# Kernel tuning notes

Hardware: AMD Instinct MI355X
Metric: run time of the kernel (lower is better)

## Reference

```python
import jax, jax.numpy as jnp
import numpy as np

SHAPES = ((92, 160), (46, 80), (23, 40), (12, 20))  # multi-scale (H, W) per level
B, NQ, C, M, P = 8, 900, 256, 8, 4
L = len(SHAPES)
D = C // M          # head dim = 32
S = sum(h * w for h, w in SHAPES)  # 19560 flattened keys
NC = 10
FFN = 1024


def setup_inputs() -> dict:
    key = jax.random.key(0)
    ks = jax.random.split(key, 16)
    f = lambda k, sh, s=0.02: jax.random.normal(k, sh, dtype=jnp.float32) * s
    return dict(
        query=jax.random.normal(ks[0], (B, NQ, C), dtype=jnp.float32),
        value=jax.random.normal(ks[1], (B, S, C), dtype=jnp.float32),
        ref_points=jax.random.uniform(ks[2], (B, NQ, 2), dtype=jnp.float32),
        w_value=f(ks[3], (C, C)), b_value=jnp.zeros((C,), jnp.float32),
        w_off=f(ks[4], (C, M * L * P * 2)), b_off=f(ks[5], (M * L * P * 2,), 0.5),
        w_attn=f(ks[6], (C, M * L * P)), b_attn=jnp.zeros((M * L * P,), jnp.float32),
        w_out=f(ks[7], (C, C)), b_out=jnp.zeros((C,), jnp.float32),
        ln1_w=jnp.ones((C,), jnp.float32), ln1_b=jnp.zeros((C,), jnp.float32),
        w_ffn1=f(ks[8], (C, FFN)), b_ffn1=jnp.zeros((FFN,), jnp.float32),
        w_ffn2=f(ks[9], (FFN, C)), b_ffn2=jnp.zeros((C,), jnp.float32),
        ln2_w=jnp.ones((C,), jnp.float32), ln2_b=jnp.zeros((C,), jnp.float32),
        w_cls=f(ks[10], (C, NC)), b_cls=jnp.zeros((NC,), jnp.float32),
    )


def _ln(x, w, b, eps=1e-6):
    u = x.mean(-1, keepdims=True)
    s = ((x - u) ** 2).mean(-1, keepdims=True)
    return (x - u) * jax.lax.rsqrt(s + eps) * w + b


def _sample_level(v_l, loc, Hl, Wl):
    # v_l: [B, Hl*Wl, M, D] level features; loc: [B, NQ, M, P, 2] normalized sampling locations.
    # Bilinear interpolation with zero padding (grid_sample align_corners=False convention).
    x = loc[..., 0] * Wl - 0.5
    y = loc[..., 1] * Hl - 0.5
    x0 = jnp.floor(x)
    y0 = jnp.floor(y)
    lx, ly = x - x0, y - y0
    vt = jnp.transpose(v_l, (0, 2, 1, 3))  # [B, M, S_l, D]

    def gather(xi, yi):
        valid = ((xi >= 0) & (xi < Wl) & (yi >= 0) & (yi < Hl)).astype(v_l.dtype)
        idx = (jnp.clip(yi, 0, Hl - 1) * Wl + jnp.clip(xi, 0, Wl - 1)).astype(jnp.int32)
        idx = jnp.transpose(idx, (0, 2, 1, 3)).reshape(B, M, NQ * P)
        g = jnp.take_along_axis(vt, idx[..., None], axis=2).reshape(B, M, NQ, P, D)
        return g * jnp.transpose(valid, (0, 2, 1, 3))[..., None]

    x0i, y0i = x0.astype(jnp.int32), y0.astype(jnp.int32)
    g00 = gather(x0i, y0i)
    g01 = gather(x0i + 1, y0i)
    g10 = gather(x0i, y0i + 1)
    g11 = gather(x0i + 1, y0i + 1)
    wx = jnp.transpose(lx, (0, 2, 1, 3))[..., None]
    wy = jnp.transpose(ly, (0, 2, 1, 3))[..., None]
    return g00 * (1 - wx) * (1 - wy) + g01 * wx * (1 - wy) + g10 * (1 - wx) * wy + g11 * wx * wy


def reference(query, value, ref_points, w_value, b_value, w_off, b_off, w_attn, b_attn,
              w_out, b_out, ln1_w, ln1_b, w_ffn1, b_ffn1, w_ffn2, b_ffn2, ln2_w, ln2_b,
              w_cls, b_cls):
    v = (value @ w_value + b_value).reshape(B, S, M, D)
    off = (query @ w_off + b_off).reshape(B, NQ, M, L, P, 2)
    attn = jax.nn.softmax((query @ w_attn + b_attn).reshape(B, NQ, M, L * P), axis=-1)
    attn = attn.reshape(B, NQ, M, L, P)
    norm = jnp.asarray([[w, h] for h, w in SHAPES], dtype=query.dtype)  # [L, 2] (W, H)
    loc = ref_points[:, :, None, None, None, :] + off / norm[None, None, None, :, None, :]

    out = jnp.zeros((B, M, NQ, D), dtype=query.dtype)
    start = 0
    for l, (Hl, Wl) in enumerate(SHAPES):
        v_l = jax.lax.dynamic_slice_in_dim(v, start, Hl * Wl, axis=1)
        samp = _sample_level(v_l, loc[:, :, :, l], Hl, Wl)          # [B, M, NQ, P, D]
        a = jnp.transpose(attn[:, :, :, l], (0, 2, 1, 3))[..., None]  # [B, M, NQ, P, 1]
        out = out + (samp * a).sum(3)
        start += Hl * Wl

    feat = jnp.transpose(out, (0, 2, 1, 3)).reshape(B, NQ, C) @ w_out + b_out
    x = _ln(query + feat, ln1_w, ln1_b)
    h = jax.nn.relu(x @ w_ffn1 + b_ffn1) @ w_ffn2 + b_ffn2
    x = _ln(x + h, ln2_w, ln2_b)
    return x @ w_cls + b_cls
```

## Files before the change

### kernel.cpp

```cpp
#include <hip/hip_runtime.h>
#include <cstddef>
#include <cstdint>

#define B_    8
#define NQ_   900
#define C_    256
#define M_    8
#define P_    4
#define L_    4
#define D_    32
#define S_    19560
#define NC_   10
#define FFN_  1024
#define RQ_   (B_ * NQ_)
#define RV_   (B_ * S_)

typedef __attribute__((ext_vector_type(8))) short bf8_t;
typedef __attribute__((ext_vector_type(8))) unsigned short us8_t;
typedef __attribute__((ext_vector_type(4))) float f4_t;
typedef unsigned short ushort_t;

__device__ __forceinline__ unsigned short f2bf(float x) {
    union { float f; unsigned u; } v; v.f = x;
    unsigned r = v.u + 0x7FFF + ((v.u >> 16) & 1);
    return (unsigned short)(r >> 16);
}
__device__ __forceinline__ float bfu2f(unsigned short u) {
    union { unsigned u; float f; } v; v.u = ((unsigned)u) << 16; return v.f;
}

__global__ __launch_bounds__(256) void prep_weights(
    const float* __restrict__ w_value, const float* __restrict__ w_off,
    const float* __restrict__ w_attn,  const float* __restrict__ w_out,
    const float* __restrict__ w_ffn1,  const float* __restrict__ w_ffn2,
    short* __restrict__ WvT, short* __restrict__ WoaT, short* __restrict__ WoutT,
    short* __restrict__ Wf1T, short* __restrict__ Wf2T)
{
    const int mat = blockIdx.z;
    int K, N; const float* src; short* dst;
    switch (mat) {
        case 0: K = 256;  N = 256;  src = w_value; dst = WvT;  break;
        case 1: K = 256;  N = 384;  src = nullptr; dst = WoaT; break;
        case 2: K = 256;  N = 256;  src = w_out;   dst = WoutT; break;
        case 3: K = 256;  N = 1024; src = w_ffn1;  dst = Wf1T; break;
        default:K = 1024; N = 256;  src = w_ffn2;  dst = Wf2T; break;
    }
    const int ntn = N >> 6;
    const int kt = blockIdx.x / ntn, nt = blockIdx.x % ntn;
    if (kt >= (K >> 6)) return;

    __shared__ float t[64][65];
    const int tx = threadIdx.x & 63;
    const int ty = threadIdx.x >> 6;
#pragma unroll
    for (int i = 0; i < 64; i += 4) {
        const int k = kt * 64 + i + ty;
        const int n = nt * 64 + tx;
        float v;
        if (mat == 1) v = (n < 256) ? w_off[(size_t)k * 256 + n]
                                    : w_attn[(size_t)k * 128 + (n - 256)];
        else          v = src[(size_t)k * N + n];
        t[i + ty][tx] = v;
    }
    __syncthreads();
#pragma unroll
    for (int i = 0; i < 64; i += 4) {
        const int n = nt * 64 + i + ty;
        const int k = kt * 64 + tx;
        dst[(size_t)n * K + k] = (short)f2bf(t[tx][i + ty]);
    }
}

__global__ __launch_bounds__(384) void prep_bias(
    const float* __restrict__ b_off, const float* __restrict__ b_attn,
    float* __restrict__ bias_cat)
{
    const int t = threadIdx.x;
    bias_cat[t] = (t < 256) ? b_off[t] : b_attn[t - 256];
}

__global__ __launch_bounds__(512, 4) void gemm_value(
    const float* __restrict__ A, const short* __restrict__ WT,
    const float* __restrict__ bias, ushort_t* __restrict__ outv, int R)
{
    __shared__ __align__(16) char smem[49152];
    short* As = (short*)smem;
    short* Bs = (short*)(smem + 16384);

    const int tid  = threadIdx.x;
    const int lane = tid & 63;
    const int wave = tid >> 6;
    const int wr   = wave >> 2;
    const int wc   = wave & 3;
    const int g    = lane >> 4;
    const int fr   = lane & 15;

    const int row0 = blockIdx.x * 128;

    const int r_base = tid >> 3;
    const int ku     = tid & 7;

    float4 rA[2][2];
#pragma unroll
    for (int it = 0; it < 2; ++it) {
        rA[it][0] = make_float4(0.f, 0.f, 0.f, 0.f);
        rA[it][1] = make_float4(0.f, 0.f, 0.f, 0.f);
    }
    int4 rB[4];
    f4_t acc[4][4] = {};

    auto LOAD = [&](int k0) {
#pragma unroll
        for (int it = 0; it < 2; ++it) {
            const int grow = row0 + it * 64 + r_base;
            if (grow < R) {
                rA[it][0] = *(const float4*)(A + (size_t)grow * 256 + k0 + ku * 8);
                rA[it][1] = *(const float4*)(A + (size_t)grow * 256 + k0 + ku * 8 + 4);
            }
        }
#pragma unroll
        for (int it = 0; it < 4; ++it) {
            const int n = it * 64 + r_base;
            rB[it] = *(const int4*)(WT + (size_t)n * 256 + k0 + ku * 8);
        }
    };
    auto WRITE = [&]() {
#pragma unroll
        for (int it = 0; it < 2; ++it) {
            const int r = it * 64 + r_base;
            const float va[8] = {rA[it][0].x, rA[it][0].y, rA[it][0].z, rA[it][0].w,
                                 rA[it][1].x, rA[it][1].y, rA[it][1].z, rA[it][1].w};
            bf8_t pk;
#pragma unroll
            for (int j = 0; j < 8; ++j) pk[j] = (short)f2bf(va[j]);
            *(bf8_t*)&As[r * 64 + (ku ^ (r & 7)) * 8] = pk;
        }
#pragma unroll
        for (int it = 0; it < 4; ++it) {
            const int n = it * 64 + r_base;
            *(int4*)&Bs[n * 64 + (ku ^ (n & 7)) * 8] = rB[it];
        }
    };

    LOAD(0);
    for (int k0 = 0; k0 < 256; k0 += 64) {
        WRITE();
        __syncthreads();
        if (k0 + 64 < 256) LOAD(k0 + 64);
#pragma unroll
        for (int c = 0; c < 2; ++c) {
            bf8_t fa[4], fb[4];
#pragma unroll
            for (int i = 0; i < 4; ++i) {
                const int ar = wr * 64 + i * 16 + fr;
                fa[i] = *(const bf8_t*)&As[ar * 64 + ((c * 4 + g) ^ (ar & 7)) * 8];
            }
#pragma unroll
            for (int j = 0; j < 4; ++j) {
                const int br = wc * 64 + j * 16 + fr;
                fb[j] = *(const bf8_t*)&Bs[br * 64 + ((c * 4 + g) ^ (br & 7)) * 8];
            }
#pragma unroll
            for (int i = 0; i < 4; ++i)
#pragma unroll
                for (int j = 0; j < 4; ++j)
                    acc[i][j] = __builtin_amdgcn_mfma_f32_16x16x32_bf16(
                        fa[i], fb[j], acc[i][j], 0, 0, 0);
        }
        __syncthreads();
    }

    ushort_t* eps = (ushort_t*)smem;
    for (int h = 0; h < 2; ++h) {
        __syncthreads();
        if ((wc >> 1) == h) {
            const int wcl = wc & 1;
#pragma unroll
            for (int j = 0; j < 4; ++j) {
                const int col_l = wcl * 64 + j * 16 + fr;
                const float bcol = bias[h * 128 + col_l];
#pragma unroll
                for (int i = 0; i < 4; ++i)
#pragma unroll
                    for (int r = 0; r < 4; ++r) {
                        const int row_l = wr * 64 + i * 16 + g * 4 + r;
                        eps[row_l * 136 + col_l] = f2bf(acc[i][j][r] + bcol);
                    }
            }
        }
        __syncthreads();
#pragma unroll
        for (int u = 0; u < 4; ++u) {
            const int unit = u * 512 + tid;
            const int sl = unit >> 4;
            const int cc = unit & 15;
            const int grow = row0 + sl;
            if (grow < R) {
                const int b = grow / S_;
                const int s = grow - b * S_;
                const int col = h * 128 + cc * 8;
                const int m = col >> 5;
                const int d = col & 31;
                *(int4*)&outv[(((size_t)(b * M_ + m)) * S_ + s) * D_ + d] =
                    *(const int4*)&eps[sl * 136 + cc * 8];
            }
        }
    }
}

template <int MODE, int BM>
__global__ __launch_bounds__(256) void gemm_mfma(
    const float* __restrict__ A, const short* __restrict__ WT,
    const float* __restrict__ bias, const float* __restrict__ res,
    float* __restrict__ out, int R, int N, int K)
{
    constexpr int NI  = BM / 32;
    constexpr int AIT = BM * 8 / 256;
    constexpr int ASB = BM * 128;
    constexpr int SMEM_BYTES = ASB + 16384;

    __shared__ __align__(16) char smem[SMEM_BYTES];
    short* As = (short*)smem;
    short* Bs = (short*)(smem + ASB);

    const int tid  = threadIdx.x;
    const int lane = tid & 63;
    const int wave = tid >> 6;
    const int wr   = wave >> 1;
    const int wc   = wave & 1;
    const int g    = lane >> 4;
    const int fr   = lane & 15;

    const int row0 = blockIdx.x * BM;
    const int col0 = blockIdx.y * 128;

    const int r_base = tid >> 3;
    const int ku     = tid & 7;

    float4 rA[AIT][2];
#pragma unroll
    for (int it = 0; it < AIT; ++it) {
        rA[it][0] = make_float4(0.f, 0.f, 0.f, 0.f);
        rA[it][1] = make_float4(0.f, 0.f, 0.f, 0.f);
    }
    int4 rB[4];

    f4_t acc[NI][4] = {};

    auto LOAD = [&](int k0) {
#pragma unroll
        for (int it = 0; it < AIT; ++it) {
            const int grow = row0 + it * 32 + r_base;
            if (grow < R) {
                rA[it][0] = *(const float4*)(A + (size_t)grow * K + k0 + ku * 8);
                rA[it][1] = *(const float4*)(A + (size_t)grow * K + k0 + ku * 8 + 4);
            }
        }
#pragma unroll
        for (int it = 0; it < 4; ++it) {
            const int n = it * 32 + r_base;
            rB[it] = *(const int4*)(WT + (size_t)(col0 + n) * K + k0 + ku * 8);
        }
    };
    auto WRITE = [&]() {
#pragma unroll
        for (int it = 0; it < AIT; ++it) {
            const int r = it * 32 + r_base;
            const float va[8] = {rA[it][0].x, rA[it][0].y, rA[it][0].z, rA[it][0].w,
                                 rA[it][1].x, rA[it][1].y, rA[it][1].z, rA[it][1].w};
            bf8_t pk;
#pragma unroll
            for (int j = 0; j < 8; ++j) pk[j] = (short)f2bf(va[j]);
            *(bf8_t*)&As[r * 64 + (ku ^ (r & 7)) * 8] = pk;
        }
#pragma unroll
        for (int it = 0; it < 4; ++it) {
            const int n = it * 32 + r_base;
            *(int4*)&Bs[n * 64 + (ku ^ (n & 7)) * 8] = rB[it];
        }
    };

    LOAD(0);
    for (int k0 = 0; k0 < K; k0 += 64) {
        WRITE();
        __syncthreads();
        if (k0 + 64 < K) LOAD(k0 + 64);
#pragma unroll
        for (int c = 0; c < 2; ++c) {
            bf8_t fa[NI], fb[4];
#pragma unroll
            for (int i = 0; i < NI; ++i) {
                const int ar = wr * (BM / 2) + i * 16 + fr;
                fa[i] = *(const bf8_t*)&As[ar * 64 + ((c * 4 + g) ^ (ar & 7)) * 8];
            }
#pragma unroll
            for (int j = 0; j < 4; ++j) {
                const int br = wc * 64 + j * 16 + fr;
                fb[j] = *(const bf8_t*)&Bs[br * 64 + ((c * 4 + g) ^ (br & 7)) * 8];
            }
#pragma unroll
            for (int i = 0; i < NI; ++i)
#pragma unroll
                for (int j = 0; j < 4; ++j)
                    acc[i][j] = __builtin_amdgcn_mfma_f32_16x16x32_bf16(
                        fa[i], fb[j], acc[i][j], 0, 0, 0);
        }
        __syncthreads();
    }

#pragma unroll
    for (int j = 0; j < 4; ++j) {
        const int col = col0 + wc * 64 + j * 16 + fr;
        const float bcol = bias[col];
#pragma unroll
        for (int i = 0; i < NI; ++i) {
#pragma unroll
            for (int r = 0; r < 4; ++r) {
                const int row = row0 + wr * (BM / 2) + i * 16 + g * 4 + r;
                if (row >= R) continue;
                float vv = acc[i][j][r] + bcol;
                if (MODE == 2) {
                    out[(size_t)row * N + col] = fmaxf(vv, 0.f);
                } else if (MODE == 3) {
                    out[(size_t)row * N + col] = vv + res[(size_t)row * N + col];
                } else {
                    out[(size_t)row * N + col] = vv;
                }
            }
        }
    }
}

__global__ __launch_bounds__(128) void softmax_loc_kernel(
    const float* __restrict__ oa, const float* __restrict__ ref,
    float* __restrict__ loc, float* __restrict__ attn)
{
    const int row = blockIdx.x;
    const int t   = threadIdx.x;
    const float Wtab[L_] = {160.f, 80.f, 40.f, 20.f};
    const float Htab[L_] = {92.f, 46.f, 23.f, 12.f};

    float vlog = oa[(size_t)row * 384 + 256 + t];
    float mx = vlog;
#pragma unroll
    for (int o = 8; o >= 1; o >>= 1) mx = fmaxf(mx, __shfl_xor(mx, o, 64));
    const float e = __expf(vlog - mx);
    float sm = e;
#pragma unroll
    for (int o = 8; o >= 1; o >>= 1) sm += __shfl_xor(sm, o, 64);
    attn[(size_t)row * 128 + t] = e / sm;

    const int m = t >> 4, l = (t >> 2) & 3, p = t & 3;
    const float rx = ref[(size_t)row * 2 + 0];
    const float ry = ref[(size_t)row * 2 + 1];
    const int oi = m * 32 + l * 8 + p * 2;
    loc[(size_t)row * 256 + oi + 0] = rx * Wtab[l] + oa[(size_t)row * 384 + oi + 0] - 0.5f;
    loc[(size_t)row * 256 + oi + 1] = ry * Htab[l] + oa[(size_t)row * 384 + oi + 1] - 0.5f;
}

__global__ __launch_bounds__(256) void sample_kernel(
    const ushort_t* __restrict__ v, const float* __restrict__ loc,
    const float* __restrict__ attn, float* __restrict__ outf)
{
    const int row0 = blockIdx.x * 8;
    const int t    = threadIdx.x;
    const int rl   = t >> 5;
    const int m    = (t >> 2) & 7;
    const int dg   = t & 3;

    __shared__ float sloc[8][8][33];
    __shared__ float satt[8][8][17];

    {
        const float4* src = (const float4*)(loc + (size_t)row0 * 256);
#pragma unroll
        for (int i = 0; i < 2; ++i) {
            const int u   = i * 256 + t;
            const int r_  = u >> 6;
            const int rem = u & 63;
            const int m_  = rem >> 3;
            const int c4  = (rem & 7) * 4;
            *(float4*)&sloc[r_][m_][c4] = src[u];
        }
        const float4* asrc = (const float4*)(attn + (size_t)row0 * 128);
        {
            const int u   = t;
            const int r_  = u >> 5;
            const int rem = u & 31;
            const int m_  = rem >> 2;
            const int c4  = (rem & 3) * 4;
            *(float4*)&satt[r_][m_][c4] = asrc[u];
        }
    }
    __syncthreads();

    const int row = row0 + rl;
    const int b   = row / NQ_;
    const ushort_t* vbase = v + (((size_t)(b * M_ + m)) * S_) * D_ + dg * 8;

    const int Wtab[L_] = {160, 80, 40, 20};
    const int Htab[L_] = {92, 46, 23, 12};
    const int Stab[L_] = {0, 14720, 18400, 19320};

    float acc[8] = {};

#pragma unroll
    for (int l = 0; l < L_; ++l) {
        const int Wl = Wtab[l], Hl = Htab[l], st = Stab[l];
#pragma unroll
        for (int p = 0; p < P_; ++p) {
            const float x = sloc[rl][m][l * 8 + p * 2 + 0];
            const float y = sloc[rl][m][l * 8 + p * 2 + 1];
            const float a = satt[rl][m][l * 4 + p];
            const float xf = floorf(x), yf = floorf(y);
            const int x0 = (int)xf, y0 = (int)yf;
            const float lx = x - xf, ly = y - yf;
            const float wx0 = (x0 >= 0 && x0 < Wl)         ? (1.f - lx) : 0.f;
            const float wx1 = (x0 + 1 >= 0 && x0 + 1 < Wl) ? lx         : 0.f;
            const float wy0 = (y0 >= 0 && y0 < Hl)         ? (1.f - ly) : 0.f;
            const float wy1 = (y0 + 1 >= 0 && y0 + 1 < Hl) ? ly         : 0.f;
            const float ay0 = a * wy0, ay1 = a * wy1;
            const float aw00 = ay0 * wx0, aw01 = ay0 * wx1;
            const float aw10 = ay1 * wx0, aw11 = ay1 * wx1;
            const int xc0 = min(max(x0, 0), Wl - 1);
            const int xc1 = min(max(x0 + 1, 0), Wl - 1);
            const int yc0 = min(max(y0, 0), Hl - 1);
            const int yc1 = min(max(y0 + 1, 0), Hl - 1);
            const us8_t s00 = *(const us8_t*)(vbase + (size_t)(st + yc0 * Wl + xc0) * D_);
            const us8_t s01 = *(const us8_t*)(vbase + (size_t)(st + yc0 * Wl + xc1) * D_);
            const us8_t s10 = *(const us8_t*)(vbase + (size_t)(st + yc1 * Wl + xc0) * D_);
            const us8_t s11 = *(const us8_t*)(vbase + (size_t)(st + yc1 * Wl + xc1) * D_);
#pragma unroll
            for (int j = 0; j < 8; ++j)
                acc[j] += aw00 * bfu2f(s00[j]) + aw01 * bfu2f(s01[j])
                        + aw10 * bfu2f(s10[j]) + aw11 * bfu2f(s11[j]);
        }
    }

    float* o = outf + (size_t)row * 256 + m * 32 + dg * 8;
    *(float4*)o       = make_float4(acc[0], acc[1], acc[2], acc[3]);
    *((float4*)o + 1) = make_float4(acc[4], acc[5], acc[6], acc[7]);
}

__global__ __launch_bounds__(64) void ln_kernel(
    const float* __restrict__ in, const float* __restrict__ w,
    const float* __restrict__ bp, float* __restrict__ out)
{
    const int row  = blockIdx.x;
    const int lane = threadIdx.x;
    const float4 x = ((const float4*)(in + (size_t)row * C_))[lane];
    float s = x.x + x.y + x.z + x.w;
#pragma unroll
    for (int o = 32; o >= 1; o >>= 1) s += __shfl_xor(s, o, 64);
    const float mean = s * (1.f / C_);
    const float d0 = x.x - mean, d1 = x.y - mean, d2 = x.z - mean, d3 = x.w - mean;
    float ss = d0 * d0 + d1 * d1 + d2 * d2 + d3 * d3;
#pragma unroll
    for (int o = 32; o >= 1; o >>= 1) ss += __shfl_xor(ss, o, 64);
    const float r = rsqrtf(ss * (1.f / C_) + 1e-6f);
    const float4 wv = ((const float4*)w)[lane];
    const float4 bv = ((const float4*)bp)[lane];
    float4 o4;
    o4.x = d0 * r * wv.x + bv.x;
    o4.y = d1 * r * wv.y + bv.y;
    o4.z = d2 * r * wv.z + bv.z;
    o4.w = d3 * r * wv.w + bv.w;
    ((float4*)(out + (size_t)row * C_))[lane] = o4;
}

__global__ __launch_bounds__(64) void cls_kernel(
    const float* __restrict__ x, const float* __restrict__ w,
    const float* __restrict__ bias, float* __restrict__ out)
{
    const int row  = blockIdx.x;
    const int lane = threadIdx.x;
    float acc[NC_] = {};
#pragma unroll
    for (int j = 0; j < 4; ++j) {
        const int k = lane + j * 64;
        const float xk = x[(size_t)row * C_ + k];
        const float* wr = w + (size_t)k * NC_;
#pragma unroll
        for (int n = 0; n < NC_; ++n) acc[n] += xk * wr[n];
    }
#pragma unroll
    for (int n = 0; n < NC_; ++n) {
        float s = acc[n];
#pragma unroll
        for (int o = 32; o >= 1; o >>= 1) s += __shfl_xor(s, o, 64);
        if (lane == n) out[(size_t)row * NC_ + n] = s + bias[n];
    }
}

extern "C" void kernel_launch(void* const* d_in, const int* in_sizes, int n_in,
                              void* d_out, int out_size, void* d_ws, size_t ws_size,
                              hipStream_t stream)
{
    const float* query   = (const float*)d_in[0];
    const float* value   = (const float*)d_in[1];
    const float* refp    = (const float*)d_in[2];
    const float* w_value = (const float*)d_in[3];
    const float* b_value = (const float*)d_in[4];
    const float* w_off   = (const float*)d_in[5];
    const float* b_off   = (const float*)d_in[6];
    const float* w_attn  = (const float*)d_in[7];
    const float* b_attn  = (const float*)d_in[8];
    const float* w_out   = (const float*)d_in[9];
    const float* b_out   = (const float*)d_in[10];
    const float* ln1w    = (const float*)d_in[11];
    const float* ln1b    = (const float*)d_in[12];
    const float* w_ffn1  = (const float*)d_in[13];
    const float* b_ffn1  = (const float*)d_in[14];
    const float* w_ffn2  = (const float*)d_in[15];
    const float* b_ffn2  = (const float*)d_in[16];
    const float* ln2w    = (const float*)d_in[17];
    const float* ln2b    = (const float*)d_in[18];
    const float* w_cls   = (const float*)d_in[19];
    const float* b_cls   = (const float*)d_in[20];

    short* WvT   = (short*)d_ws;
    short* WoaT  = WvT  + 65536;
    short* WoutT = WoaT + 98304;
    short* Wf1T  = WoutT + 65536;
    short* Wf2T  = Wf1T + 262144;
    float* bias_cat = (float*)(Wf2T + 262144);
    ushort_t* v = (ushort_t*)(bias_cat + 384);
    float* oa   = (float*)(v + (size_t)RV_ * C_);
    float* loc  = oa   + (size_t)RQ_ * 384;
    float* attn = loc  + (size_t)RQ_ * 256;
    float* feat = attn + (size_t)RQ_ * 128;
    float* tmp  = feat + (size_t)RQ_ * 256;
    float* h    = tmp  + (size_t)RQ_ * 256;
    float* x2   = h    + (size_t)RQ_ * FFN_;

    prep_weights<<<dim3(64, 1, 5), 256, 0, stream>>>(
        w_value, w_off, w_attn, w_out, w_ffn1, w_ffn2,
        WvT, WoaT, WoutT, Wf1T, Wf2T);
    prep_bias<<<1, 384, 0, stream>>>(b_off, b_attn, bias_cat);

    gemm_value<<<(RV_ + 127) / 128, 512, 0, stream>>>(
        value, WvT, b_value, v, RV_);

    gemm_mfma<0, 64><<<dim3((RQ_ + 63) / 64, 3), 256, 0, stream>>>(
        query, WoaT, bias_cat, nullptr, oa, RQ_, 384, 256);

    softmax_loc_kernel<<<RQ_, 128, 0, stream>>>(oa, refp, loc, attn);

    sample_kernel<<<RQ_ / 8, 256, 0, stream>>>(v, loc, attn, feat);

    gemm_mfma<3, 64><<<dim3((RQ_ + 63) / 64, 2), 256, 0, stream>>>(
        feat, WoutT, b_out, query, tmp, RQ_, 256, 256);

    ln_kernel<<<RQ_, 64, 0, stream>>>(tmp, ln1w, ln1b, feat);

    gemm_mfma<2, 64><<<dim3((RQ_ + 63) / 64, 8), 256, 0, stream>>>(
        feat, Wf1T, b_ffn1, nullptr, h, RQ_, 1024, 256);

    gemm_mfma<3, 64><<<dim3((RQ_ + 63) / 64, 2), 256, 0, stream>>>(
        h, Wf2T, b_ffn2, feat, tmp, RQ_, 256, 1024);

    ln_kernel<<<RQ_, 64, 0, stream>>>(tmp, ln2w, ln2b, x2);

    cls_kernel<<<RQ_, 64, 0, stream>>>(x2, w_cls, b_cls, (float*)d_out);
}
```

Baseline: 493.6 us.

## Shrink value GEMM tile to 64 rows with double-buffered A prefetch

The value-projection GEMM now uses 64-row tiles instead of 128, which halves the A shared-memory buffer and the accumulator count, and raises the occupancy hint to 6 blocks. The K loop is fully unrolled, and A loads are prefetched two stages ahead into alternating register buffers. The epilogue writes the whole 256-column tile at once, without the two-half pass. This targets better latency hiding and occupancy on the memory-bound value GEMM, at the cost of more loads of B per row and removing the row bounds check on A loads (RV is divisible by 64).

```diff
diff --git a/kernel.cpp b/kernel.cpp
--- a/kernel.cpp
+++ b/kernel.cpp
@@ -79,13 +79,13 @@
     bias_cat[t] = (t < 256) ? b_off[t] : b_attn[t - 256];
 }
 
-__global__ __launch_bounds__(512, 4) void gemm_value(
+__global__ __launch_bounds__(512, 6) void gemm_value(
     const float* __restrict__ A, const short* __restrict__ WT,
     const float* __restrict__ bias, ushort_t* __restrict__ outv, int R)
 {
-    __shared__ __align__(16) char smem[49152];
+    __shared__ __align__(16) char smem[40960];
     short* As = (short*)smem;
-    short* Bs = (short*)(smem + 16384);
+    short* Bs = (short*)(smem + 8192);
 
     const int tid  = threadIdx.x;
     const int lane = tid & 63;
@@ -95,64 +95,50 @@
     const int g    = lane >> 4;
     const int fr   = lane & 15;
 
-    const int row0 = blockIdx.x * 128;
-
-    const int r_base = tid >> 3;
-    const int ku     = tid & 7;
-
-    float4 rA[2][2];
-#pragma unroll
-    for (int it = 0; it < 2; ++it) {
-        rA[it][0] = make_float4(0.f, 0.f, 0.f, 0.f);
-        rA[it][1] = make_float4(0.f, 0.f, 0.f, 0.f);
-    }
+    const int row0 = blockIdx.x * 64;
+
+    const int rb = tid >> 3;
+    const int ku = tid & 7;
+
+    const float* Arow = A + (size_t)(row0 + rb) * 256 + ku * 8;
+
+    float4 rA0[2], rA1[2];
     int4 rB[4];
-    f4_t acc[4][4] = {};
-
-    auto LOAD = [&](int k0) {
-#pragma unroll
-        for (int it = 0; it < 2; ++it) {
-            const int grow = row0 + it * 64 + r_base;
-            if (grow < R) {
-                rA[it][0] = *(const float4*)(A + (size_t)grow * 256 + k0 + ku * 8);
-                rA[it][1] = *(const float4*)(A + (size_t)grow * 256 + k0 + ku * 8 + 4);
-            }
-        }
+    f4_t acc[2][4] = {};
+
+    auto LOADA = [&](float4* dst, int k0) {
+        dst[0] = *(const float4*)(Arow + k0);
+        dst[1] = *(const float4*)(Arow + k0 + 4);
+    };
+    auto LOADB = [&](int k0) {
 #pragma unroll
         for (int it = 0; it < 4; ++it) {
-            const int n = it * 64 + r_base;
+            const int n = it * 64 + rb;
             rB[it] = *(const int4*)(WT + (size_t)n * 256 + k0 + ku * 8);
         }
     };
-    auto WRITE = [&]() {
-#pragma unroll
-        for (int it = 0; it < 2; ++it) {
-            const int r = it * 64 + r_base;
-            const float va[8] = {rA[it][0].x, rA[it][0].y, rA[it][0].z, rA[it][0].w,
-                                 rA[it][1].x, rA[it][1].y, rA[it][1].z, rA[it][1].w};
-            bf8_t pk;
-#pragma unroll
-            for (int j = 0; j < 8; ++j) pk[j] = (short)f2bf(va[j]);
-            *(bf8_t*)&As[r * 64 + (ku ^ (r & 7)) * 8] = pk;
-        }
+    auto WRITEA = [&](const float4* src) {
+        const float va[8] = {src[0].x, src[0].y, src[0].z, src[0].w,
+                             src[1].x, src[1].y, src[1].z, src[1].w};
+        bf8_t pk;
+#pragma unroll
+        for (int j = 0; j < 8; ++j) pk[j] = (short)f2bf(va[j]);
+        *(bf8_t*)&As[rb * 64 + (ku ^ (rb & 7)) * 8] = pk;
+    };
+    auto WRITEB = [&]() {
 #pragma unroll
         for (int it = 0; it < 4; ++it) {
-            const int n = it * 64 + r_base;
+            const int n = it * 64 + rb;
             *(int4*)&Bs[n * 64 + (ku ^ (n & 7)) * 8] = rB[it];
         }
     };
-
-    LOAD(0);
-    for (int k0 = 0; k0 < 256; k0 += 64) {
-        WRITE();
-        __syncthreads();
-        if (k0 + 64 < 256) LOAD(k0 + 64);
+    auto MFMA = [&]() {
 #pragma unroll
         for (int c = 0; c < 2; ++c) {
-            bf8_t fa[4], fb[4];
-#pragma unroll
-            for (int i = 0; i < 4; ++i) {
-                const int ar = wr * 64 + i * 16 + fr;
+            bf8_t fa[2], fb[4];
+#pragma unroll
+            for (int i = 0; i < 2; ++i) {
+                const int ar = wr * 32 + i * 16 + fr;
                 fa[i] = *(const bf8_t*)&As[ar * 64 + ((c * 4 + g) ^ (ar & 7)) * 8];
             }
 #pragma unroll
@@ -161,49 +147,62 @@
                 fb[j] = *(const bf8_t*)&Bs[br * 64 + ((c * 4 + g) ^ (br & 7)) * 8];
             }
 #pragma unroll
-            for (int i = 0; i < 4; ++i)
+            for (int i = 0; i < 2; ++i)
 #pragma unroll
                 for (int j = 0; j < 4; ++j)
                     acc[i][j] = __builtin_amdgcn_mfma_f32_16x16x32_bf16(
                         fa[i], fb[j], acc[i][j], 0, 0, 0);
         }
-        __syncthreads();
-    }
+    };
+
+    LOADA(rA0, 0); LOADA(rA1, 64); LOADB(0);
+    WRITEA(rA0); WRITEB();
+    __syncthreads();
+    LOADB(64); LOADA(rA0, 128);
+    MFMA();
+    __syncthreads();
+    WRITEA(rA1); WRITEB();
+    __syncthreads();
+    LOADB(128); LOADA(rA1, 192);
+    MFMA();
+    __syncthreads();
+    WRITEA(rA0); WRITEB();
+    __syncthreads();
+    LOADB(192);
+    MFMA();
+    __syncthreads();
+    WRITEA(rA1); WRITEB();
+    __syncthreads();
+    MFMA();
+    __syncthreads();
 
     ushort_t* eps = (ushort_t*)smem;
-    for (int h = 0; h < 2; ++h) {
-        __syncthreads();
-        if ((wc >> 1) == h) {
-            const int wcl = wc & 1;
-#pragma unroll
-            for (int j = 0; j < 4; ++j) {
-                const int col_l = wcl * 64 + j * 16 + fr;
-                const float bcol = bias[h * 128 + col_l];
-#pragma unroll
-                for (int i = 0; i < 4; ++i)
-#pragma unroll
-                    for (int r = 0; r < 4; ++r) {
-                        const int row_l = wr * 64 + i * 16 + g * 4 + r;
-                        eps[row_l * 136 + col_l] = f2bf(acc[i][j][r] + bcol);
-                    }
-            }
-        }
-        __syncthreads();
-#pragma unroll
-        for (int u = 0; u < 4; ++u) {
-            const int unit = u * 512 + tid;
-            const int sl = unit >> 4;
-            const int cc = unit & 15;
-            const int grow = row0 + sl;
-            if (grow < R) {
-                const int b = grow / S_;
-                const int s = grow - b * S_;
-                const int col = h * 128 + cc * 8;
-                const int m = col >> 5;
-                const int d = col & 31;
-                *(int4*)&outv[(((size_t)(b * M_ + m)) * S_ + s) * D_ + d] =
-                    *(const int4*)&eps[sl * 136 + cc * 8];
-            }
+#pragma unroll
+    for (int j = 0; j < 4; ++j) {
+        const int col_l = wc * 64 + j * 16 + fr;
+        const float bcol = bias[col_l];
+#pragma unroll
+        for (int i = 0; i < 2; ++i)
+#pragma unroll
+            for (int r = 0; r < 4; ++r) {
+                const int row_l = wr * 32 + i * 16 + g * 4 + r;
+                eps[row_l * 264 + col_l] = f2bf(acc[i][j][r] + bcol);
+            }
+    }
+    __syncthreads();
+#pragma unroll
+    for (int u = 0; u < 4; ++u) {
+        const int unit = u * 512 + tid;
+        const int sl = unit >> 5;
+        const int cc = unit & 31;
+        const int grow = row0 + sl;
+        if (grow < R) {
+            const int b = grow / S_;
+            const int s = grow - b * S_;
+            const int m = cc >> 2;
+            const int d = (cc & 3) * 8;
+            *(int4*)&outv[(((size_t)(b * M_ + m)) * S_ + s) * D_ + d] =
+                *(const int4*)&eps[sl * 264 + cc * 8];
         }
     }
 }
@@ -538,7 +537,7 @@
         WvT, WoaT, WoutT, Wf1T, Wf2T);
     prep_bias<<<1, 384, 0, stream>>>(b_off, b_attn, bias_cat);
 
-    gemm_value<<<(RV_ + 127) / 128, 512, 0, stream>>>(
+    gemm_value<<<RV_ / 64, 512, 0, stream>>>(
         value, WvT, b_value, v, RV_);
 
     gemm_mfma<0, 64><<<dim3((RQ_ + 63) / 64, 3), 256, 0, stream>>>(
```

New measurement: 566.4 us. +14.7%, slower.
